# Optimization experiments

Hardware: AMD Instinct MI355X
Metric: run time of the kernel (lower is better)

The kernel has to match this reference:

```python
import jax, jax.numpy as jnp
import numpy as np
import math

DEPTH = 3
NUM_GRAPHS = 8
BN_EPS = 1e-5
POOL_RATIO = 0.5


def _gcn(A, x, W, b):
    # GCNConv(improved=True): A_hat = A + 2*I; out = D^-1/2 A_hat D^-1/2 (x W) + b
    n = A.shape[0]
    A_hat = A + 2.0 * jnp.eye(n, dtype=A.dtype)
    deg = A_hat.sum(axis=1)
    d = jnp.where(deg > 0, jax.lax.rsqrt(deg), 0.0)
    return d[:, None] * (A_hat @ (d[:, None] * (x @ W))) + b


def _bn_eval(x, g, b):
    # BatchNorm1d in eval mode with running_mean=0, running_var=1
    return x * (g / jnp.sqrt(1.0 + BN_EPS)) + b


def _forward(x, edge_index, batch, conv0_w, conv0_b, down_w, down_b, pool_w,
             up_w, up_b, lins_w, lins_b, bn_g, bn_b, out_w, out_b):
    n0 = x.shape[0]
    # dense weighted adjacency A[dst, src] += 1 (duplicates sum, same as scatter-add MP)
    A = jnp.zeros((n0, n0), x.dtype).at[edge_index[1], edge_index[0]].add(1.0)

    # ---- GraphUNet (eval mode: dropout p=0.92 is identity) ----
    h = jax.nn.relu(_gcn(A, x, conv0_w, conv0_b))
    xs, As, perms = [h], [A], []
    for i in range(DEPTH):
        n = A.shape[0]
        eye = jnp.eye(n, dtype=A.dtype)
        S = A + eye                       # add_self_loops(weight=1)
        A2 = (S @ S) * (1.0 - eye)        # spspmm then remove_self_loops
        # TopKPooling: score = tanh((x.w)/||w||), keep top ceil(0.5*n) nodes
        score = jnp.tanh((h @ pool_w[i]) / jnp.linalg.norm(pool_w[i]))
        k = math.ceil(POOL_RATIO * n)
        _, perm = jax.lax.top_k(score, k)
        h = h[perm] * score[perm][:, None]
        A = A2[perm][:, perm]             # filter_adj
        h = jax.nn.relu(_gcn(A, h, down_w[i], down_b[i]))
        if i < DEPTH - 1:
            xs.append(h)
            As.append(A)
        perms.append(perm)
    for i in range(DEPTH):
        j = DEPTH - 1 - i
        res, Aj, perm = xs[j], As[j], perms[j]
        up = jnp.zeros_like(res).at[perm].set(h)
        h = res + up                      # sum_res=True skip connection
        h = _gcn(Aj, h, up_w[i], up_b[i])
        if i < DEPTH - 1:
            h = jax.nn.relu(h)

    # ---- global_add_pool + BN/Linear/tanh head ----
    g = jax.ops.segment_sum(h, batch, num_segments=NUM_GRAPHS)
    for i in range(3):
        g = _bn_eval(g, bn_g[i], bn_b[i])
        g = jnp.tanh(g @ lins_w[i] + lins_b[i])
    g = _bn_eval(g, bn_g[3], bn_b[3])
    return g @ out_w + out_b


def setup_inputs() -> dict:
    key = jax.random.key(0)
    ks = jax.random.split(key, 20)
    N, F, H, O, E = 4096, 64, 128, 32, 65536
    s = 0.05
    x = jax.random.normal(ks[0], (N, F), jnp.float32)
    src = jax.random.randint(ks[1], (E,), 0, N)
    dst = jax.random.randint(ks[2], (E,), 0, N)
    edge_index = jnp.stack([jnp.concatenate([src, dst]),
                            jnp.concatenate([dst, src])]).astype(jnp.int32)
    batch = jnp.sort(jax.random.randint(ks[3], (N,), 0, NUM_GRAPHS)).astype(jnp.int32)
    return {
        "x": x,
        "edge_index": edge_index,
        "batch": batch,
        "conv0_w": jax.random.normal(ks[4], (F, H), jnp.float32) * s,
        "conv0_b": jnp.zeros((H,), jnp.float32),
        "down_w": jax.random.normal(ks[5], (DEPTH, H, H), jnp.float32) * s,
        "down_b": jnp.zeros((DEPTH, H), jnp.float32),
        "pool_w": jax.random.normal(ks[6], (DEPTH, H), jnp.float32),
        "up_w": jax.random.normal(ks[7], (DEPTH, H, H), jnp.float32) * s,
        "up_b": jnp.zeros((DEPTH, H), jnp.float32),
        "lins_w": jax.random.normal(ks[8], (3, H, H), jnp.float32) * s,
        "lins_b": jnp.zeros((3, H), jnp.float32),
        "bn_g": jnp.ones((4, H), jnp.float32),
        "bn_b": jnp.zeros((4, H), jnp.float32),
        "out_w": jax.random.normal(ks[9], (H, O), jnp.float32) * s,
        "out_b": jnp.zeros((O,), jnp.float32),
    }


def reference(x, edge_index, batch, conv0_w, conv0_b, down_w, down_b, pool_w,
              up_w, up_b, lins_w, lins_b, bn_g, bn_b, out_w, out_b):
    return _forward(x, edge_index, batch, conv0_w, conv0_b, down_w, down_b,
                    pool_w, up_w, up_b, lins_w, lins_b, bn_g, bn_b, out_w, out_b)
```

## Files before the change

kernel.cpp:

```cpp
#include <hip/hip_runtime.h>
#include <math.h>

#define H 128
#define NG 8

typedef __attribute__((ext_vector_type(8))) short bf16x8;
typedef __attribute__((ext_vector_type(8))) unsigned short ushort8;
typedef __attribute__((ext_vector_type(4))) float f32x4;

static __device__ __forceinline__ float b2f(unsigned short u) {
  union { unsigned int i; float f; } v;
  v.i = ((unsigned int)u) << 16;
  return v.f;
}
static __device__ __forceinline__ unsigned short f2b(float f) {
  return (unsigned short)(__float_as_uint(f) >> 16);
}

__global__ void k_hist(const int* __restrict__ ei, int E, int* __restrict__ cnt) {
  int e = blockIdx.x * 256 + threadIdx.x;
  if (e >= E) return;
  atomicAdd(&cnt[ei[E + e]], 1);
}

__global__ __launch_bounds__(1024) void k_scan(const int* __restrict__ cnt,
                                               int* __restrict__ rowptr,
                                               float* __restrict__ dv, int n) {
  __shared__ int sums[1024];
  int tid = threadIdx.x;
  int base = tid * 4;
  int v0 = 0, v1 = 0, v2 = 0, v3 = 0;
  if (base < n) { v0 = cnt[base]; v1 = cnt[base + 1]; v2 = cnt[base + 2]; v3 = cnt[base + 3]; }
  int s = v0 + v1 + v2 + v3;
  sums[tid] = s;
  __syncthreads();
  for (int off = 1; off < 1024; off <<= 1) {
    int t = (tid >= off) ? sums[tid - off] : 0;
    __syncthreads();
    sums[tid] += t;
    __syncthreads();
  }
  int excl = sums[tid] - s;
  if (base < n) {
    rowptr[base] = excl;
    rowptr[base + 1] = excl + v0;
    rowptr[base + 2] = excl + v0 + v1;
    rowptr[base + 3] = excl + v0 + v1 + v2;
    dv[base] = rsqrtf((float)v0 + 2.0f);
    dv[base + 1] = rsqrtf((float)v1 + 2.0f);
    dv[base + 2] = rsqrtf((float)v2 + 2.0f);
    dv[base + 3] = rsqrtf((float)v3 + 2.0f);
  }
  if (tid == 1023) rowptr[n] = sums[1023];
}

__global__ void k_fill(const int* __restrict__ ei, int E, const int* __restrict__ rowptr,
                       int* __restrict__ cursor, int* __restrict__ colidx) {
  int e = blockIdx.x * 256 + threadIdx.x;
  if (e >= E) return;
  int r = ei[E + e], c = ei[e];
  int p = atomicAdd(&cursor[r], 1);
  colidx[rowptr[r] + p] = c;
}

__global__ void k_deg(const float* __restrict__ A, int n, float* __restrict__ dv) {
  int row = blockIdx.x * (blockDim.x >> 6) + (threadIdx.x >> 6);
  int lane = threadIdx.x & 63;
  if (row >= n) return;
  float s = 0.f;
  const float* arow = A + (size_t)row * n;
  for (int j = lane; j < n; j += 64) s += arow[j];
#pragma unroll
  for (int o = 32; o > 0; o >>= 1) s += __shfl_down(s, o);
  if (lane == 0) dv[row] = rsqrtf(s + 2.0f);
}

template <int MODE, int RS>
__global__ __launch_bounds__(256) void k_xw(const float* __restrict__ X,
                                            const float* __restrict__ W,
                                            const float* __restrict__ dv,
                                            const int* __restrict__ idx,
                                            const float* __restrict__ aux,
                                            float* __restrict__ Y, int n, int F) {
  __shared__ float Xs[64][36];
  __shared__ float Ws[32][132];
  __shared__ int ridx[64];
  __shared__ float rscl[64];
  int tid = threadIdx.x;
  int rowBase = blockIdx.x * 64;
  if (MODE == 1) {
    if (tid < 64) {
      int pp = idx[rowBase + tid];
      ridx[tid] = pp;
      rscl[tid] = aux[pp];
    }
  } else if (MODE == 2) {
    if (tid < 64) ridx[tid] = idx[rowBase + tid];
  }
  if (MODE != 0) __syncthreads();
  int r0 = (tid >> 5) << 3;
  int c0 = (tid & 31) << 2;
  float acc[8][4] = {};
  for (int k0 = 0; k0 < F; k0 += 32) {
#pragma unroll
    for (int it = 0, e = tid; it < 8; ++it, e += 256) {
      int ii = e >> 5, kk = e & 31;
      int gk = k0 + kk;
      float v;
      if (MODE == 0) {
        v = X[(size_t)(rowBase + ii) * F + gk];
      } else if (MODE == 1) {
        v = X[(size_t)ridx[ii] * F + gk] * rscl[ii];
      } else {
        v = X[(size_t)(rowBase + ii) * F + gk];
        int iv = ridx[ii];
        if (iv >= 0) v += aux[(size_t)iv * H + gk];
      }
      Xs[ii][kk] = v;
    }
#pragma unroll
    for (int it = 0, e = tid; it < 4; ++it, e += 256) {
      int kk = e >> 5, cc4 = e & 31;
      *(float4*)&Ws[kk][cc4 << 2] = *(const float4*)&W[(size_t)(k0 + kk) * H + (cc4 << 2)];
    }
    __syncthreads();
#pragma unroll
    for (int kk = 0; kk < 32; kk += 4) {
      float4 a4[8], w4[4];
#pragma unroll
      for (int i = 0; i < 8; ++i) a4[i] = *(const float4*)&Xs[r0 + i][kk];
#pragma unroll
      for (int s = 0; s < 4; ++s) w4[s] = *(const float4*)&Ws[kk + s][c0];
#pragma unroll
      for (int i = 0; i < 8; ++i) {
        float av[4] = {a4[i].x, a4[i].y, a4[i].z, a4[i].w};
#pragma unroll
        for (int s = 0; s < 4; ++s) {
          float wv[4] = {w4[s].x, w4[s].y, w4[s].z, w4[s].w};
#pragma unroll
          for (int j = 0; j < 4; ++j) acc[i][j] = fmaf(av[s], wv[j], acc[i][j]);
        }
      }
    }
    __syncthreads();
  }
#pragma unroll
  for (int i = 0; i < 8; ++i) {
    int row = rowBase + r0 + i;
    float d = RS ? rsqrtf(dv[row] + 2.0f) : dv[row];
    *(float4*)&Y[(size_t)row * H + c0] =
        make_float4(d * acc[i][0], d * acc[i][1], d * acc[i][2], d * acc[i][3]);
  }
}

__global__ void k_spmm_fin(const int* __restrict__ rowptr, const int* __restrict__ colidx,
                           const float* __restrict__ Y, const float* __restrict__ dv,
                           const float* __restrict__ bias, float* __restrict__ Out,
                           int n, int relu) {
  int row = blockIdx.x * 4 + (threadIdx.x >> 6);
  int lane = threadIdx.x & 63;
  if (row >= n) return;
  int s = rowptr[row], e = rowptr[row + 1];
  int c2 = lane * 2;
  float a0 = 0.f, a1 = 0.f;
  int i = s;
  for (; i + 1 < e; i += 2) {
    int cA = colidx[i], cB = colidx[i + 1];
    float2 yA = *(const float2*)&Y[(size_t)cA * H + c2];
    float2 yB = *(const float2*)&Y[(size_t)cB * H + c2];
    a0 += yA.x + yB.x;
    a1 += yA.y + yB.y;
  }
  if (i < e) {
    int c = colidx[i];
    float2 y = *(const float2*)&Y[(size_t)c * H + c2];
    a0 += y.x;
    a1 += y.y;
  }
  float d = dv[row];
  float2 yr = *(const float2*)&Y[(size_t)row * H + c2];
  float v0 = d * (a0 + 2.0f * yr.x) + bias[c2];
  float v1 = d * (a1 + 2.0f * yr.y) + bias[c2 + 1];
  if (relu) { v0 = fmaxf(v0, 0.f); v1 = fmaxf(v1, 0.f); }
  float2 o = make_float2(v0, v1);
  *(float2*)&Out[(size_t)row * H + c2] = o;
}

__global__ __launch_bounds__(256) void k_ata_rows(const int* __restrict__ rowptr,
                                                  const int* __restrict__ colidx,
                                                  const int* __restrict__ perm,
                                                  const int* __restrict__ inv,
                                                  unsigned short* __restrict__ Ab,
                                                  float* __restrict__ dv, int kdim) {
  __shared__ int acc[2048];
  __shared__ int wsum[4];
  int i = blockIdx.x;
  int tid = threadIdx.x;
  for (int j = tid; j < kdim; j += 256) acc[j] = 0;
  __syncthreads();
  int p = perm[i];
  int s = rowptr[p], e = rowptr[p + 1];
  int deg = e - s;
  int wave = tid >> 6, lane = tid & 63;
  for (int q = wave; q <= deg; q += 4) {
    int kn = (q < deg) ? colidx[s + q] : p;
    int s2 = rowptr[kn], e2 = rowptr[kn + 1];
    for (int idx = s2 + lane; idx <= e2; idx += 64) {
      int j = (idx < e2) ? colidx[idx] : kn;
      int ii = inv[j];
      if (ii >= 0) atomicAdd(&acc[ii], 1);
    }
  }
  __syncthreads();
  int rs = 0;
  {
    int j0 = tid * 8;
    ushort8 v;
#pragma unroll
    for (int q = 0; q < 8; ++q) {
      int j = j0 + q;
      int c = (j == i) ? 0 : acc[j];
      rs += c;
      v[q] = f2b((float)c);
    }
    *(ushort8*)&Ab[(size_t)i * kdim + j0] = v;
  }
#pragma unroll
  for (int o = 32; o > 0; o >>= 1) rs += __shfl_down(rs, o);
  if (lane == 0) wsum[wave] = rs;
  __syncthreads();
  if (tid == 0) dv[i] = rsqrtf((float)(wsum[0] + wsum[1] + wsum[2] + wsum[3]) + 2.0f);
}

__global__ __launch_bounds__(256) void k_ata_mfma_g(const unsigned short* __restrict__ Ab,
                                                    const int* __restrict__ perm,
                                                    float* __restrict__ PartC,
                                                    int n, int k, int KC) {
  __shared__ __align__(16) unsigned short As[64][64];
  __shared__ __align__(16) unsigned short Bs[64][64];
  __shared__ int pr[64], pc[64];
  int tid = threadIdx.x;
  int w = tid >> 6, ln = tid & 63;
  int l15 = ln & 15, l4 = ln >> 4;
  int br = blockIdx.y, bc = blockIdx.x;
  if (tid < 64) pr[tid] = perm[br * 64 + tid];
  else if (tid < 128) pc[tid - 64] = perm[bc * 64 + (tid - 64)];
  __syncthreads();
  f32x4 acc[4] = {};
  int k0s = blockIdx.z * KC;
  for (int k0 = k0s; k0 < k0s + KC; k0 += 64) {
#pragma unroll
    for (int it = 0; it < 2; ++it) {
      int e = tid + it * 256;
      int row = e >> 3, ch = e & 7;
      int sch = (ch ^ (row & 7)) * 8;
      int base = k0 + ch * 8;
      {
        int p = pr[row];
        ushort8 v = *(const ushort8*)&Ab[(size_t)p * n + base];
#pragma unroll
        for (int q = 0; q < 8; ++q)
          if (base + q == p) v[q] = f2b(b2f(v[q]) + 1.0f);
        *(ushort8*)&As[row][sch] = v;
      }
      {
        int p = pc[row];
        ushort8 v = *(const ushort8*)&Ab[(size_t)p * n + base];
#pragma unroll
        for (int q = 0; q < 8; ++q)
          if (base + q == p) v[q] = f2b(b2f(v[q]) + 1.0f);
        *(ushort8*)&Bs[row][sch] = v;
      }
    }
    __syncthreads();
#pragma unroll
    for (int s = 0; s < 2; ++s) {
      int arow = w * 16 + l15;
      bf16x8 af = *(const bf16x8*)&As[arow][((s * 4 + l4) ^ (arow & 7)) * 8];
#pragma unroll
      for (int f = 0; f < 4; ++f) {
        int brow = f * 16 + l15;
        bf16x8 bfr = *(const bf16x8*)&Bs[brow][((s * 4 + l4) ^ (brow & 7)) * 8];
        acc[f] = __builtin_amdgcn_mfma_f32_16x16x32_bf16(af, bfr, acc[f], 0, 0, 0);
      }
    }
    __syncthreads();
  }
  float* out = PartC + (size_t)blockIdx.z * k * k;
#pragma unroll
  for (int f = 0; f < 4; ++f) {
#pragma unroll
    for (int r = 0; r < 4; ++r) {
      int gi = br * 64 + w * 16 + l4 * 4 + r;
      int gj = bc * 64 + f * 16 + l15;
      out[(size_t)gi * k + gj] = acc[f][r];
    }
  }
}

__global__ __launch_bounds__(256) void k_ata_fin(const float* __restrict__ PartC,
                                                 float* __restrict__ C,
                                                 float* __restrict__ rowsum, int k) {
  __shared__ float wsum[4];
  int gi = blockIdx.x;
  int tid = threadIdx.x;
  int j4 = tid * 4;
  size_t stride = (size_t)k * k;
  size_t off = (size_t)gi * k + j4;
  float4 s = *(const float4*)&PartC[off];
#pragma unroll
  for (int z = 1; z < 4; ++z) {
    float4 p = *(const float4*)&PartC[z * stride + off];
    s.x += p.x; s.y += p.y; s.z += p.z; s.w += p.w;
  }
  if (gi >= j4 && gi < j4 + 4) ((float*)&s)[gi - j4] = 0.0f;
  *(float4*)&C[off] = s;
  float part = s.x + s.y + s.z + s.w;
  int lane = tid & 63, wave = tid >> 6;
#pragma unroll
  for (int o = 32; o > 0; o >>= 1) part += __shfl_down(part, o);
  if (lane == 0) wsum[wave] = part;
  __syncthreads();
  if (tid == 0) rowsum[gi] = wsum[0] + wsum[1] + wsum[2] + wsum[3];
}

__global__ void k_cvt_split(const float* __restrict__ Y, unsigned short* __restrict__ YT, int n) {
  int c = blockIdx.x;
  for (int k0 = threadIdx.x * 8; k0 < n; k0 += 256 * 8) {
    ushort8 hi, lo;
#pragma unroll
    for (int q = 0; q < 8; ++q) {
      float v = Y[(size_t)(k0 + q) * H + c];
      unsigned short h = f2b(v);
      hi[q] = h;
      lo[q] = f2b(v - b2f(h));
    }
    *(ushort8*)&YT[(size_t)c * (2 * n) + k0] = hi;
    *(ushort8*)&YT[(size_t)c * (2 * n) + n + k0] = lo;
  }
}

__global__ __launch_bounds__(256) void k_gcn_mfma(const unsigned short* __restrict__ A,
                                                  const unsigned short* __restrict__ YT,
                                                  float* __restrict__ Part, int n, int VK) {
  __shared__ __align__(16) unsigned short As[64][64];
  __shared__ __align__(16) unsigned short Bs[128][64];
  int tid = threadIdx.x;
  int w = tid >> 6, ln = tid & 63;
  int l15 = ln & 15, l4 = ln >> 4;
  int rowBase = blockIdx.x * 64;
  float* out = Part + (size_t)blockIdx.y * n * H;
  f32x4 acc[8] = {};
  int vk0s = blockIdx.y * VK;
  for (int vk0 = vk0s; vk0 < vk0s + VK; vk0 += 64) {
    int ka = vk0 & (n - 1);
#pragma unroll
    for (int it = 0; it < 2; ++it) {
      int e = tid + it * 256;
      int row = e >> 3, ch = e & 7;
      int sch = (ch ^ (row & 7)) * 8;
      *(ushort8*)&As[row][sch] = *(const ushort8*)&A[(size_t)(rowBase + row) * n + ka + ch * 8];
    }
#pragma unroll
    for (int it = 0; it < 4; ++it) {
      int e = tid + it * 256;
      int row = e >> 3, ch = e & 7;
      int sch = (ch ^ (row & 7)) * 8;
      *(ushort8*)&Bs[row][sch] = *(const ushort8*)&YT[(size_t)row * (2 * n) + vk0 + ch * 8];
    }
    __syncthreads();
#pragma unroll
    for (int s = 0; s < 2; ++s) {
      int arow = w * 16 + l15;
      bf16x8 af = *(const bf16x8*)&As[arow][((s * 4 + l4) ^ (arow & 7)) * 8];
#pragma unroll
      for (int f = 0; f < 8; ++f) {
        int brow = f * 16 + l15;
        bf16x8 bfr = *(const bf16x8*)&Bs[brow][((s * 4 + l4) ^ (brow & 7)) * 8];
        acc[f] = __builtin_amdgcn_mfma_f32_16x16x32_bf16(af, bfr, acc[f], 0, 0, 0);
      }
    }
    __syncthreads();
  }
#pragma unroll
  for (int f = 0; f < 8; ++f) {
#pragma unroll
    for (int r = 0; r < 4; ++r) {
      int row = rowBase + w * 16 + l4 * 4 + r;
      out[(size_t)row * H + f * 16 + l15] = acc[f][r];
    }
  }
}

__global__ __launch_bounds__(256) void k_ata_sk(const float* __restrict__ A,
                                                const int* __restrict__ perm,
                                                float* __restrict__ C, int n, int k, int CK) {
  int bc = blockIdx.x, br = blockIdx.y;
  if (br > bc) return;
  __shared__ float As[64][36];
  __shared__ float Bs[64][36];
  __shared__ int pr[64], pc[64];
  int tid = threadIdx.x;
  if (tid < 64) pr[tid] = perm[br * 64 + tid];
  else if (tid < 128) pc[tid - 64] = perm[bc * 64 + (tid - 64)];
  __syncthreads();
  int ty = tid >> 4;
  int tx = tid & 15;
  float acc[4][4] = {};
  int k0s = blockIdx.z * CK;
  for (int k0 = k0s; k0 < k0s + CK; k0 += 32) {
#pragma unroll
    for (int it = 0, e = tid; it < 8; ++it, e += 256) {
      int ii = e >> 5, kk = e & 31;
      int gk = k0 + kk;
      int p = pr[ii];
      As[ii][kk] = A[(size_t)p * n + gk] + ((p == gk) ? 1.0f : 0.0f);
      p = pc[ii];
      Bs[ii][kk] = A[(size_t)p * n + gk] + ((p == gk) ? 1.0f : 0.0f);
    }
    __syncthreads();
#pragma unroll
    for (int kk = 0; kk < 32; kk += 4) {
      float4 a4[4], b4[4];
#pragma unroll
      for (int i = 0; i < 4; ++i) a4[i] = *(const float4*)&As[ty + 16 * i][kk];
#pragma unroll
      for (int j = 0; j < 4; ++j) b4[j] = *(const float4*)&Bs[tx + 16 * j][kk];
#pragma unroll
      for (int i = 0; i < 4; ++i) {
        float av[4] = {a4[i].x, a4[i].y, a4[i].z, a4[i].w};
#pragma unroll
        for (int j = 0; j < 4; ++j) {
          float bv[4] = {b4[j].x, b4[j].y, b4[j].z, b4[j].w};
#pragma unroll
          for (int s = 0; s < 4; ++s) acc[i][j] = fmaf(av[s], bv[s], acc[i][j]);
        }
      }
    }
    __syncthreads();
  }
  bool diag = (br == bc);
#pragma unroll
  for (int i = 0; i < 4; ++i) {
    int gi = br * 64 + ty + 16 * i;
#pragma unroll
    for (int j = 0; j < 4; ++j) {
      int gj = bc * 64 + tx + 16 * j;
      if (gi == gj) continue;
      float v = acc[i][j];
      atomicAdd(&C[(size_t)gi * k + gj], v);
      if (!diag) atomicAdd(&C[(size_t)gj * k + gi], v);
    }
  }
}

__global__ __launch_bounds__(256) void k_gcn_part(const float* __restrict__ A,
                                                  const float* __restrict__ Y,
                                                  float* __restrict__ Part,
                                                  int n, int KC) {
  __shared__ float As[64][36];
  __shared__ float Ys[32][132];
  int tid = threadIdx.x;
  int r0 = (tid >> 5) << 3;
  int c0 = (tid & 31) << 2;
  size_t rowBase = (size_t)blockIdx.x * 64;
  int k0s = blockIdx.y * KC;
  float* out = Part + (size_t)blockIdx.y * n * H;
  float acc[8][4] = {};
  for (int k0 = k0s; k0 < k0s + KC; k0 += 32) {
#pragma unroll
    for (int it = 0, e = tid; it < 8; ++it, e += 256) {
      int ii = e >> 5, kk = e & 31;
      As[ii][kk] = A[(rowBase + ii) * (size_t)n + k0 + kk];
    }
#pragma unroll
    for (int it = 0, e = tid; it < 4; ++it, e += 256) {
      int kk = e >> 5, cc4 = e & 31;
      *(float4*)&Ys[kk][cc4 << 2] = *(const float4*)&Y[(size_t)(k0 + kk) * H + (cc4 << 2)];
    }
    __syncthreads();
#pragma unroll
    for (int kk = 0; kk < 32; kk += 4) {
      float4 a4[8], y4[4];
#pragma unroll
      for (int i = 0; i < 8; ++i) a4[i] = *(const float4*)&As[r0 + i][kk];
#pragma unroll
      for (int s = 0; s < 4; ++s) y4[s] = *(const float4*)&Ys[kk + s][c0];
#pragma unroll
      for (int i = 0; i < 8; ++i) {
        float av[4] = {a4[i].x, a4[i].y, a4[i].z, a4[i].w};
#pragma unroll
        for (int s = 0; s < 4; ++s) {
          float yv[4] = {y4[s].x, y4[s].y, y4[s].z, y4[s].w};
#pragma unroll
          for (int j = 0; j < 4; ++j) acc[i][j] = fmaf(av[s], yv[j], acc[i][j]);
        }
      }
    }
    __syncthreads();
  }
#pragma unroll
  for (int i = 0; i < 8; ++i) {
    size_t row = rowBase + r0 + i;
    *(float4*)&out[row * H + c0] = make_float4(acc[i][0], acc[i][1], acc[i][2], acc[i][3]);
  }
}

template <int RS>
__global__ void k_gcn_fin(const float* __restrict__ Part, const float* __restrict__ Y,
                          const float* __restrict__ dv, const float* __restrict__ bias,
                          float* __restrict__ Out, int n, int nch, int relu) {
  int i4 = blockIdx.x * 256 + threadIdx.x;
  if (i4 * 4 >= n * H) return;
  int row = i4 >> 5, c4 = (i4 & 31) * 4;
  size_t stride = (size_t)n * H;
  float4 s = *(const float4*)&Part[i4 * 4];
  for (int c = 1; c < nch; ++c) {
    float4 p = *(const float4*)&Part[c * stride + i4 * 4];
    s.x += p.x; s.y += p.y; s.z += p.z; s.w += p.w;
  }
  float4 y = *(const float4*)&Y[i4 * 4];
  float d = RS ? rsqrtf(dv[row] + 2.0f) : dv[row];
  float4 v;
  v.x = d * (s.x + 2.0f * y.x) + bias[c4];
  v.y = d * (s.y + 2.0f * y.y) + bias[c4 + 1];
  v.z = d * (s.z + 2.0f * y.z) + bias[c4 + 2];
  v.w = d * (s.w + 2.0f * y.w) + bias[c4 + 3];
  if (relu) {
    v.x = fmaxf(v.x, 0.f); v.y = fmaxf(v.y, 0.f);
    v.z = fmaxf(v.z, 0.f); v.w = fmaxf(v.w, 0.f);
  }
  *(float4*)&Out[i4 * 4] = v;
}

__global__ void k_score(const float* __restrict__ h, const float* __restrict__ w,
                        float* __restrict__ score, int n) {
  __shared__ float wn;
  int tid = threadIdx.x;
  if (tid < 64) {
    float s = w[tid] * w[tid] + w[tid + 64] * w[tid + 64];
#pragma unroll
    for (int o = 32; o > 0; o >>= 1) s += __shfl_down(s, o);
    if (tid == 0) wn = sqrtf(s);
  }
  __syncthreads();
  int row = blockIdx.x * 4 + (tid >> 6);
  int lane = tid & 63;
  if (row >= n) return;
  float s = h[(size_t)row * H + lane] * w[lane] + h[(size_t)row * H + lane + 64] * w[lane + 64];
#pragma unroll
  for (int o = 32; o > 0; o >>= 1) s += __shfl_down(s, o);
  if (lane == 0) score[row] = tanhf(s / wn);
}

static __device__ __forceinline__ void ce_(unsigned long long& x, unsigned long long& y, bool asc) {
  if ((x < y) != asc) { unsigned long long t = x; x = y; y = t; }
}
static __device__ __forceinline__ unsigned long long pick_(unsigned long long a,
                                                           unsigned long long b,
                                                           bool lower, bool asc) {
  unsigned long long lo = (a < b) ? a : b;
  unsigned long long hi = (a < b) ? b : a;
  return (lower == asc) ? lo : hi;
}

template <int LOGN>
__global__ __launch_bounds__(1024) void k_topk(const float* __restrict__ score,
                                               int* __restrict__ perm,
                                               int* __restrict__ inv) {
  const int n = 1 << LOGN;
  __shared__ unsigned long long lds[1 << LOGN];
  int t = threadIdx.x;
  int e0 = t * 4;
  unsigned long long key[4];
#pragma unroll
  for (int j = 0; j < 4; ++j) {
    unsigned u = __float_as_uint(score[e0 + j]);
    u = (u & 0x80000000u) ? ~u : (u | 0x80000000u);
    u = ~u;
    key[j] = (((unsigned long long)u) << 32) | (unsigned)(e0 + j);
  }
  ce_(key[0], key[1], true);
  ce_(key[2], key[3], false);
  for (int size = 4; size <= n; size <<= 1) {
    bool asc = ((e0 & size) == 0);
    for (int stride = size >> 1; stride >= 256; stride >>= 1) {
#pragma unroll
      for (int j = 0; j < 4; ++j) lds[e0 + j] = key[j];
      __syncthreads();
      bool lower = ((e0 & stride) == 0);
#pragma unroll
      for (int j = 0; j < 4; ++j)
        key[j] = pick_(key[j], lds[(e0 + j) ^ stride], lower, asc);
      __syncthreads();
    }
    int s0 = ((size >> 1) < 256) ? (size >> 1) : 128;
    for (int stride = s0; stride >= 4; stride >>= 1) {
      int m = stride >> 2;
      bool lower = ((t & m) == 0);
#pragma unroll
      for (int j = 0; j < 4; ++j) {
        unsigned long long o = __shfl_xor(key[j], m, 64);
        key[j] = pick_(key[j], o, lower, asc);
      }
    }
    ce_(key[0], key[2], asc);
    ce_(key[1], key[3], asc);
    ce_(key[0], key[1], asc);
    ce_(key[2], key[3], asc);
  }
  int kk = n >> 1;
#pragma unroll
  for (int j = 0; j < 4; ++j) {
    int e = e0 + j;
    int idx = (int)(key[j] & 0xffffffffu);
    if (e < kk) perm[e] = idx;
    if (inv) inv[idx] = (e < kk) ? e : -1;
  }
}

__global__ void k_segsum(const float* __restrict__ h, const int* __restrict__ batch,
                         float* __restrict__ g, int n) {
  int c = threadIdx.x;
  int r0 = blockIdx.x * 32;
  int rend = min(r0 + 32, n);
  float acc = 0.f;
  int cur = batch[r0];
  for (int r = r0; r < rend; ++r) {
    int b = batch[r];
    if (b != cur) { atomicAdd(&g[cur * H + c], acc); acc = 0.f; cur = b; }
    acc += h[(size_t)r * H + c];
  }
  atomicAdd(&g[cur * H + c], acc);
}

__global__ __launch_bounds__(256) void k_head(const float* __restrict__ g,
    const float* __restrict__ lins_w, const float* __restrict__ lins_b,
    const float* __restrict__ bn_g, const float* __restrict__ bn_b,
    const float* __restrict__ out_w, const float* __restrict__ out_b,
    float* __restrict__ out) {
  __shared__ float a[NG * H], b[NG * H];
  int tid = threadIdx.x;
  const float inv = 1.0f / sqrtf(1.0f + 1e-5f);
  for (int i = tid; i < NG * H; i += 256) a[i] = g[i];
  __syncthreads();
  for (int L = 0; L < 3; ++L) {
    for (int i = tid; i < NG * H; i += 256) {
      int c = i & 127;
      b[i] = a[i] * (bn_g[L * H + c] * inv) + bn_b[L * H + c];
    }
    __syncthreads();
    for (int i = tid; i < NG * H; i += 256) {
      int r = i >> 7, c = i & 127;
      float s = lins_b[L * H + c];
      for (int k2 = 0; k2 < H; ++k2) s += b[r * H + k2] * lins_w[(size_t)L * H * H + k2 * H + c];
      a[i] = tanhf(s);
    }
    __syncthreads();
  }
  for (int i = tid; i < NG * H; i += 256) {
    int c = i & 127;
    b[i] = a[i] * (bn_g[3 * H + c] * inv) + bn_b[3 * H + c];
  }
  __syncthreads();
  for (int i = tid; i < NG * 32; i += 256) {
    int r = i >> 5, o = i & 31;
    float s = out_b[o];
    for (int k2 = 0; k2 < H; ++k2) s += b[r * H + k2] * out_w[k2 * 32 + o];
    out[i] = s;
  }
}

extern "C" void kernel_launch(void* const* d_in, const int* in_sizes, int n_in,
                              void* d_out, int out_size, void* d_ws, size_t ws_size,
                              hipStream_t stream) {
  const float* x       = (const float*)d_in[0];
  const int*   ei      = (const int*)d_in[1];
  const int*   batch   = (const int*)d_in[2];
  const float* conv0_w = (const float*)d_in[3];
  const float* conv0_b = (const float*)d_in[4];
  const float* down_w  = (const float*)d_in[5];
  const float* down_b  = (const float*)d_in[6];
  const float* pool_w  = (const float*)d_in[7];
  const float* up_w    = (const float*)d_in[8];
  const float* up_b    = (const float*)d_in[9];
  const float* lins_w  = (const float*)d_in[10];
  const float* lins_b  = (const float*)d_in[11];
  const float* bn_g    = (const float*)d_in[12];
  const float* bn_b    = (const float*)d_in[13];
  const float* out_w   = (const float*)d_in[14];
  const float* out_b   = (const float*)d_in[15];
  int E = in_sizes[1] / 2;

  char* p = (char*)d_ws;
  auto alloc = [&](size_t bytes) {
    char* r = p;
    p += (bytes + 255) & ~(size_t)255;
    return r;
  };
  unsigned short* A1b  = (unsigned short*)alloc((size_t)2048 * 2048 * 2);
  unsigned short* YT   = (unsigned short*)alloc((size_t)128 * 4096 * 2);
  float*          A2m  = (float*)alloc((size_t)1024 * 1024 * 4);
  float*          A3   = (float*)alloc((size_t)512 * 512 * 4);
  float*          part = (float*)alloc((size_t)16 * 1024 * 1024 * 4);
  int* cnt    = (int*)alloc(4096 * 4);
  int* cursor = (int*)alloc(4096 * 4);
  int* rowptr = (int*)alloc(4100 * 4);
  int* colidx = (int*)alloc((size_t)E * 4);
  int* inv0   = (int*)alloc(4096 * 4);
  int* inv1   = (int*)alloc(2048 * 4);
  int* inv2   = (int*)alloc(1024 * 4);
  float* dv0  = (float*)alloc(4096 * 4);
  float* dv1  = (float*)alloc(2048 * 4);
  float* dv2  = (float*)alloc(1024 * 4);
  float* dv3  = (float*)alloc(512 * 4);
  int* perm0  = (int*)alloc(2048 * 4);
  int* perm1  = (int*)alloc(1024 * 4);
  int* perm2  = (int*)alloc(512 * 4);
  float* score = (float*)alloc(4096 * 4);
  float* h0 = (float*)alloc((size_t)4096 * H * 4);
  float* h1 = (float*)alloc((size_t)2048 * H * 4);
  float* h2 = (float*)alloc((size_t)1024 * H * 4);
  float* h3 = (float*)alloc((size_t)512 * H * 4);
  float* t2 = (float*)alloc((size_t)4096 * H * 4);
  float* hu = (float*)alloc((size_t)4096 * H * 4);
  float* g  = (float*)alloc(NG * H * 4);

  auto gcn = [&](const float* A, const float* Y, const float* dvv, const float* bias,
                 float* Out, int nn, int relu, bool rs) {
    const int nch = 8;
    int KC = nn / nch;
    k_gcn_part<<<dim3(nn / 64, nch), 256, 0, stream>>>(A, Y, part, nn, KC);
    if (rs)
      k_gcn_fin<1><<<nn / 8, 256, 0, stream>>>(part, Y, dvv, bias, Out, nn, nch, relu);
    else
      k_gcn_fin<0><<<nn / 8, 256, 0, stream>>>(part, Y, dvv, bias, Out, nn, nch, relu);
  };
  auto gcn_mfma = [&](const unsigned short* Ab, const float* Y, const float* dvv,
                      const float* bias, float* Out, int nn, int relu) {
    k_cvt_split<<<128, 256, 0, stream>>>(Y, YT, nn);
    k_gcn_mfma<<<dim3(nn / 64, 16), 256, 0, stream>>>(Ab, YT, part, nn, (2 * nn) / 16);
    k_gcn_fin<0><<<nn / 8, 256, 0, stream>>>(part, Y, dvv, bias, Out, nn, 16, relu);
  };

  hipMemsetAsync(cnt, 0, 4096 * 4, stream);
  hipMemsetAsync(cursor, 0, 4096 * 4, stream);
  k_hist<<<(E + 255) / 256, 256, 0, stream>>>(ei, E, cnt);
  k_scan<<<1, 1024, 0, stream>>>(cnt, rowptr, dv0, 4096);
  k_fill<<<(E + 255) / 256, 256, 0, stream>>>(ei, E, rowptr, cursor, colidx);

  k_xw<0, 0><<<4096 / 64, 256, 0, stream>>>(x, conv0_w, dv0, nullptr, nullptr, t2, 4096, 64);
  k_spmm_fin<<<1024, 256, 0, stream>>>(rowptr, colidx, t2, dv0, conv0_b, h0, 4096, 1);

  k_score<<<1024, 256, 0, stream>>>(h0, pool_w, score, 4096);
  k_topk<12><<<1, 1024, 0, stream>>>(score, perm0, inv0);
  k_ata_rows<<<2048, 256, 0, stream>>>(rowptr, colidx, perm0, inv0, A1b, dv1, 2048);
  k_xw<1, 0><<<2048 / 64, 256, 0, stream>>>(h0, down_w, dv1, perm0, score, t2, 2048, 128);
  gcn_mfma(A1b, t2, dv1, down_b, h1, 2048, 1);

  k_score<<<512, 256, 0, stream>>>(h1, pool_w + H, score, 2048);
  k_topk<11><<<1, 512, 0, stream>>>(score, perm1, inv1);
  k_ata_mfma_g<<<dim3(16, 16, 4), 256, 0, stream>>>(A1b, perm1, part, 2048, 1024, 512);
  k_ata_fin<<<1024, 256, 0, stream>>>(part, A2m, dv2, 1024);
  k_xw<1, 1><<<1024 / 64, 256, 0, stream>>>(h1, down_w + (size_t)H * H, dv2, perm1, score, t2, 1024, 128);
  gcn(A2m, t2, dv2, down_b + H, h2, 1024, 1, true);

  k_score<<<256, 256, 0, stream>>>(h2, pool_w + 2 * H, score, 1024);
  k_topk<10><<<1, 256, 0, stream>>>(score, perm2, inv2);
  hipMemsetAsync(A3, 0, (size_t)512 * 512 * 4, stream);
  k_ata_sk<<<dim3(8, 8, 8), 256, 0, stream>>>(A2m, perm2, A3, 1024, 512, 128);
  k_deg<<<512 / 4, 256, 0, stream>>>(A3, 512, dv3);
  k_xw<1, 0><<<512 / 64, 256, 0, stream>>>(h2, down_w + (size_t)2 * H * H, dv3, perm2, score, t2, 512, 128);
  gcn(A3, t2, dv3, down_b + 2 * H, h3, 512, 1, false);

  k_xw<2, 1><<<1024 / 64, 256, 0, stream>>>(h2, up_w, dv2, inv2, h3, t2, 1024, 128);
  gcn(A2m, t2, dv2, up_b, hu, 1024, 1, true);

  k_xw<2, 0><<<2048 / 64, 256, 0, stream>>>(h1, up_w + (size_t)H * H, dv1, inv1, hu, t2, 2048, 128);
  gcn_mfma(A1b, t2, dv1, up_b + H, hu, 2048, 1);

  k_xw<2, 0><<<4096 / 64, 256, 0, stream>>>(h0, up_w + (size_t)2 * H * H, dv0, inv0, hu, t2, 4096, 128);
  k_spmm_fin<<<1024, 256, 0, stream>>>(rowptr, colidx, t2, dv0, up_b + 2 * H, hu, 4096, 0);

  hipMemsetAsync(g, 0, NG * H * 4, stream);
  k_segsum<<<4096 / 32, 128, 0, stream>>>(hu, batch, g, 4096);
  k_head<<<1, 256, 0, stream>>>(g, lins_w, lins_b, bn_g, bn_b, out_w, out_b, (float*)d_out);
}
```

Baseline: 512.0 us.

## Fuse score into GCN epilogues, emit bf16 split in xw, replace atomic ATA with partials

```diff
diff --git a/kernel.cpp b/kernel.cpp
--- a/kernel.cpp
+++ b/kernel.cpp
@@ -63,25 +63,15 @@
   colidx[rowptr[r] + p] = c;
 }
 
-__global__ void k_deg(const float* __restrict__ A, int n, float* __restrict__ dv) {
-  int row = blockIdx.x * (blockDim.x >> 6) + (threadIdx.x >> 6);
-  int lane = threadIdx.x & 63;
-  if (row >= n) return;
-  float s = 0.f;
-  const float* arow = A + (size_t)row * n;
-  for (int j = lane; j < n; j += 64) s += arow[j];
-#pragma unroll
-  for (int o = 32; o > 0; o >>= 1) s += __shfl_down(s, o);
-  if (lane == 0) dv[row] = rsqrtf(s + 2.0f);
-}
-
-template <int MODE, int RS>
+template <int MODE, int RS, int EMIT>
 __global__ __launch_bounds__(256) void k_xw(const float* __restrict__ X,
                                             const float* __restrict__ W,
                                             const float* __restrict__ dv,
                                             const int* __restrict__ idx,
                                             const float* __restrict__ aux,
-                                            float* __restrict__ Y, int n, int F) {
+                                            float* __restrict__ Y,
+                                            unsigned short* __restrict__ YT,
+                                            int n, int F) {
   __shared__ float Xs[64][36];
   __shared__ float Ws[32][132];
   __shared__ int ridx[64];
@@ -144,21 +134,53 @@
     }
     __syncthreads();
   }
+  float vout[8][4];
 #pragma unroll
   for (int i = 0; i < 8; ++i) {
     int row = rowBase + r0 + i;
     float d = RS ? rsqrtf(dv[row] + 2.0f) : dv[row];
+#pragma unroll
+    for (int j = 0; j < 4; ++j) vout[i][j] = d * acc[i][j];
     *(float4*)&Y[(size_t)row * H + c0] =
-        make_float4(d * acc[i][0], d * acc[i][1], d * acc[i][2], d * acc[i][3]);
-  }
-}
-
+        make_float4(vout[i][0], vout[i][1], vout[i][2], vout[i][3]);
+  }
+  if (EMIT) {
+#pragma unroll
+    for (int j = 0; j < 4; ++j) {
+      ushort8 hi, lo;
+#pragma unroll
+      for (int i = 0; i < 8; ++i) {
+        float v = vout[i][j];
+        unsigned short hh = f2b(v);
+        hi[i] = hh;
+        lo[i] = f2b(v - b2f(hh));
+      }
+      int c = c0 + j;
+      *(ushort8*)&YT[(size_t)c * (2 * n) + rowBase + r0] = hi;
+      *(ushort8*)&YT[(size_t)c * (2 * n) + n + rowBase + r0] = lo;
+    }
+  }
+}
+
+template <int SCORE>
 __global__ void k_spmm_fin(const int* __restrict__ rowptr, const int* __restrict__ colidx,
                            const float* __restrict__ Y, const float* __restrict__ dv,
                            const float* __restrict__ bias, float* __restrict__ Out,
+                           const float* __restrict__ w, float* __restrict__ score,
                            int n, int relu) {
-  int row = blockIdx.x * 4 + (threadIdx.x >> 6);
-  int lane = threadIdx.x & 63;
+  __shared__ float wn;
+  int tid = threadIdx.x;
+  if (SCORE) {
+    if (tid < 64) {
+      float s = w[tid] * w[tid] + w[tid + 64] * w[tid + 64];
+#pragma unroll
+      for (int o = 32; o > 0; o >>= 1) s += __shfl_down(s, o);
+      if (tid == 0) wn = sqrtf(s);
+    }
+    __syncthreads();
+  }
+  int row = blockIdx.x * 4 + (tid >> 6);
+  int lane = tid & 63;
   if (row >= n) return;
   int s = rowptr[row], e = rowptr[row + 1];
   int c2 = lane * 2;
@@ -182,8 +204,13 @@
   float v0 = d * (a0 + 2.0f * yr.x) + bias[c2];
   float v1 = d * (a1 + 2.0f * yr.y) + bias[c2 + 1];
   if (relu) { v0 = fmaxf(v0, 0.f); v1 = fmaxf(v1, 0.f); }
-  float2 o = make_float2(v0, v1);
-  *(float2*)&Out[(size_t)row * H + c2] = o;
+  *(float2*)&Out[(size_t)row * H + c2] = make_float2(v0, v1);
+  if (SCORE) {
+    float sc = v0 * w[c2] + v1 * w[c2 + 1];
+#pragma unroll
+    for (int o = 32; o > 0; o >>= 1) sc += __shfl_down(sc, o);
+    if (lane == 0) score[row] = tanhf(sc / wn);
+  }
 }
 
 __global__ __launch_bounds__(256) void k_ata_rows(const int* __restrict__ rowptr,
@@ -298,9 +325,68 @@
   }
 }
 
-__global__ __launch_bounds__(256) void k_ata_fin(const float* __restrict__ PartC,
-                                                 float* __restrict__ C,
-                                                 float* __restrict__ rowsum, int k) {
+__global__ __launch_bounds__(256) void k_ata_sk_part(const float* __restrict__ A,
+                                                     const int* __restrict__ perm,
+                                                     float* __restrict__ PartC,
+                                                     int n, int k, int CK) {
+  int bc = blockIdx.x, br = blockIdx.y;
+  __shared__ float As[64][36];
+  __shared__ float Bs[64][36];
+  __shared__ int pr[64], pc[64];
+  int tid = threadIdx.x;
+  if (tid < 64) pr[tid] = perm[br * 64 + tid];
+  else if (tid < 128) pc[tid - 64] = perm[bc * 64 + (tid - 64)];
+  __syncthreads();
+  int ty = tid >> 4;
+  int tx = tid & 15;
+  float acc[4][4] = {};
+  int k0s = blockIdx.z * CK;
+  for (int k0 = k0s; k0 < k0s + CK; k0 += 32) {
+#pragma unroll
+    for (int it = 0, e = tid; it < 8; ++it, e += 256) {
+      int ii = e >> 5, kk = e & 31;
+      int gk = k0 + kk;
+      int p = pr[ii];
+      As[ii][kk] = A[(size_t)p * n + gk] + ((p == gk) ? 1.0f : 0.0f);
+      p = pc[ii];
+      Bs[ii][kk] = A[(size_t)p * n + gk] + ((p == gk) ? 1.0f : 0.0f);
+    }
+    __syncthreads();
+#pragma unroll
+    for (int kk = 0; kk < 32; kk += 4) {
+      float4 a4[4], b4[4];
+#pragma unroll
+      for (int i = 0; i < 4; ++i) a4[i] = *(const float4*)&As[ty + 16 * i][kk];
+#pragma unroll
+      for (int j = 0; j < 4; ++j) b4[j] = *(const float4*)&Bs[tx + 16 * j][kk];
+#pragma unroll
+      for (int i = 0; i < 4; ++i) {
+        float av[4] = {a4[i].x, a4[i].y, a4[i].z, a4[i].w};
+#pragma unroll
+        for (int j = 0; j < 4; ++j) {
+          float bv[4] = {b4[j].x, b4[j].y, b4[j].z, b4[j].w};
+#pragma unroll
+          for (int s = 0; s < 4; ++s) acc[i][j] = fmaf(av[s], bv[s], acc[i][j]);
+        }
+      }
+    }
+    __syncthreads();
+  }
+  float* out = PartC + (size_t)blockIdx.z * k * k;
+#pragma unroll
+  for (int i = 0; i < 4; ++i) {
+    int gi = br * 64 + ty + 16 * i;
+#pragma unroll
+    for (int j = 0; j < 4; ++j) {
+      int gj = bc * 64 + tx + 16 * j;
+      out[(size_t)gi * k + gj] = acc[i][j];
+    }
+  }
+}
+
+template <int NCH>
+__global__ void k_ata_fin(const float* __restrict__ PartC, float* __restrict__ C,
+                          float* __restrict__ rowsum, int k) {
   __shared__ float wsum[4];
   int gi = blockIdx.x;
   int tid = threadIdx.x;
@@ -309,7 +395,7 @@
   size_t off = (size_t)gi * k + j4;
   float4 s = *(const float4*)&PartC[off];
 #pragma unroll
-  for (int z = 1; z < 4; ++z) {
+  for (int z = 1; z < NCH; ++z) {
     float4 p = *(const float4*)&PartC[z * stride + off];
     s.x += p.x; s.y += p.y; s.z += p.z; s.w += p.w;
   }
@@ -321,22 +407,11 @@
   for (int o = 32; o > 0; o >>= 1) part += __shfl_down(part, o);
   if (lane == 0) wsum[wave] = part;
   __syncthreads();
-  if (tid == 0) rowsum[gi] = wsum[0] + wsum[1] + wsum[2] + wsum[3];
-}
-
-__global__ void k_cvt_split(const float* __restrict__ Y, unsigned short* __restrict__ YT, int n) {
-  int c = blockIdx.x;
-  for (int k0 = threadIdx.x * 8; k0 < n; k0 += 256 * 8) {
-    ushort8 hi, lo;
-#pragma unroll
-    for (int q = 0; q < 8; ++q) {
-      float v = Y[(size_t)(k0 + q) * H + c];
-      unsigned short h = f2b(v);
-      hi[q] = h;
-      lo[q] = f2b(v - b2f(h));
-    }
-    *(ushort8*)&YT[(size_t)c * (2 * n) + k0] = hi;
-    *(ushort8*)&YT[(size_t)c * (2 * n) + n + k0] = lo;
+  if (tid == 0) {
+    int nw = blockDim.x >> 6;
+    float t = 0.f;
+    for (int q = 0; q < nw; ++q) t += wsum[q];
+    rowsum[gi] = t;
   }
 }
 
@@ -392,68 +467,6 @@
   }
 }
 
-__global__ __launch_bounds__(256) void k_ata_sk(const float* __restrict__ A,
-                                                const int* __restrict__ perm,
-                                                float* __restrict__ C, int n, int k, int CK) {
-  int bc = blockIdx.x, br = blockIdx.y;
-  if (br > bc) return;
-  __shared__ float As[64][36];
-  __shared__ float Bs[64][36];
-  __shared__ int pr[64], pc[64];
-  int tid = threadIdx.x;
-  if (tid < 64) pr[tid] = perm[br * 64 + tid];
-  else if (tid < 128) pc[tid - 64] = perm[bc * 64 + (tid - 64)];
-  __syncthreads();
-  int ty = tid >> 4;
-  int tx = tid & 15;
-  float acc[4][4] = {};
-  int k0s = blockIdx.z * CK;
-  for (int k0 = k0s; k0 < k0s + CK; k0 += 32) {
-#pragma unroll
-    for (int it = 0, e = tid; it < 8; ++it, e += 256) {
-      int ii = e >> 5, kk = e & 31;
-      int gk = k0 + kk;
-      int p = pr[ii];
-      As[ii][kk] = A[(size_t)p * n + gk] + ((p == gk) ? 1.0f : 0.0f);
-      p = pc[ii];
-      Bs[ii][kk] = A[(size_t)p * n + gk] + ((p == gk) ? 1.0f : 0.0f);
-    }
-    __syncthreads();
-#pragma unroll
-    for (int kk = 0; kk < 32; kk += 4) {
-      float4 a4[4], b4[4];
-#pragma unroll
-      for (int i = 0; i < 4; ++i) a4[i] = *(const float4*)&As[ty + 16 * i][kk];
-#pragma unroll
-      for (int j = 0; j < 4; ++j) b4[j] = *(const float4*)&Bs[tx + 16 * j][kk];
-#pragma unroll
-      for (int i = 0; i < 4; ++i) {
-        float av[4] = {a4[i].x, a4[i].y, a4[i].z, a4[i].w};
-#pragma unroll
-        for (int j = 0; j < 4; ++j) {
-          float bv[4] = {b4[j].x, b4[j].y, b4[j].z, b4[j].w};
-#pragma unroll
-          for (int s = 0; s < 4; ++s) acc[i][j] = fmaf(av[s], bv[s], acc[i][j]);
-        }
-      }
-    }
-    __syncthreads();
-  }
-  bool diag = (br == bc);
-#pragma unroll
-  for (int i = 0; i < 4; ++i) {
-    int gi = br * 64 + ty + 16 * i;
-#pragma unroll
-    for (int j = 0; j < 4; ++j) {
-      int gj = bc * 64 + tx + 16 * j;
-      if (gi == gj) continue;
-      float v = acc[i][j];
-      atomicAdd(&C[(size_t)gi * k + gj], v);
-      if (!diag) atomicAdd(&C[(size_t)gj * k + gi], v);
-    }
-  }
-}
-
 __global__ __launch_bounds__(256) void k_gcn_part(const float* __restrict__ A,
                                                   const float* __restrict__ Y,
                                                   float* __restrict__ Part,
@@ -506,12 +519,24 @@
   }
 }
 
-template <int RS>
+template <int RS, int SCORE>
 __global__ void k_gcn_fin(const float* __restrict__ Part, const float* __restrict__ Y,
                           const float* __restrict__ dv, const float* __restrict__ bias,
-                          float* __restrict__ Out, int n, int nch, int relu) {
-  int i4 = blockIdx.x * 256 + threadIdx.x;
-  if (i4 * 4 >= n * H) return;
+                          float* __restrict__ Out,
+                          const float* __restrict__ w, float* __restrict__ score,
+                          int n, int nch, int relu) {
+  __shared__ float wn;
+  int tid = threadIdx.x;
+  if (SCORE) {
+    if (tid < 64) {
+      float s = w[tid] * w[tid] + w[tid + 64] * w[tid + 64];
+#pragma unroll
+      for (int o = 32; o > 0; o >>= 1) s += __shfl_down(s, o);
+      if (tid == 0) wn = sqrtf(s);
+    }
+    __syncthreads();
+  }
+  int i4 = blockIdx.x * 256 + tid;
   int row = i4 >> 5, c4 = (i4 & 31) * 4;
   size_t stride = (size_t)n * H;
   float4 s = *(const float4*)&Part[i4 * 4];
@@ -531,26 +556,12 @@
     v.z = fmaxf(v.z, 0.f); v.w = fmaxf(v.w, 0.f);
   }
   *(float4*)&Out[i4 * 4] = v;
-}
-
-__global__ void k_score(const float* __restrict__ h, const float* __restrict__ w,
-                        float* __restrict__ score, int n) {
-  __shared__ float wn;
-  int tid = threadIdx.x;
-  if (tid < 64) {
-    float s = w[tid] * w[tid] + w[tid + 64] * w[tid + 64];
-#pragma unroll
-    for (int o = 32; o > 0; o >>= 1) s += __shfl_down(s, o);
-    if (tid == 0) wn = sqrtf(s);
-  }
-  __syncthreads();
-  int row = blockIdx.x * 4 + (tid >> 6);
-  int lane = tid & 63;
-  if (row >= n) return;
-  float s = h[(size_t)row * H + lane] * w[lane] + h[(size_t)row * H + lane + 64] * w[lane + 64];
-#pragma unroll
-  for (int o = 32; o > 0; o >>= 1) s += __shfl_down(s, o);
-  if (lane == 0) score[row] = tanhf(s / wn);
+  if (SCORE) {
+    float sc = v.x * w[c4] + v.y * w[c4 + 1] + v.z * w[c4 + 2] + v.w * w[c4 + 3];
+#pragma unroll
+    for (int o = 16; o > 0; o >>= 1) sc += __shfl_down(sc, o, 32);
+    if ((tid & 31) == 0) score[row] = tanhf(sc / wn);
+  }
 }
 
 static __device__ __forceinline__ void ce_(unsigned long long& x, unsigned long long& y, bool asc) {
@@ -726,61 +737,44 @@
   float* hu = (float*)alloc((size_t)4096 * H * 4);
   float* g  = (float*)alloc(NG * H * 4);
 
-  auto gcn = [&](const float* A, const float* Y, const float* dvv, const float* bias,
-                 float* Out, int nn, int relu, bool rs) {
-    const int nch = 8;
-    int KC = nn / nch;
-    k_gcn_part<<<dim3(nn / 64, nch), 256, 0, stream>>>(A, Y, part, nn, KC);
-    if (rs)
-      k_gcn_fin<1><<<nn / 8, 256, 0, stream>>>(part, Y, dvv, bias, Out, nn, nch, relu);
-    else
-      k_gcn_fin<0><<<nn / 8, 256, 0, stream>>>(part, Y, dvv, bias, Out, nn, nch, relu);
-  };
-  auto gcn_mfma = [&](const unsigned short* Ab, const float* Y, const float* dvv,
-                      const float* bias, float* Out, int nn, int relu) {
-    k_cvt_split<<<128, 256, 0, stream>>>(Y, YT, nn);
-    k_gcn_mfma<<<dim3(nn / 64, 16), 256, 0, stream>>>(Ab, YT, part, nn, (2 * nn) / 16);
-    k_gcn_fin<0><<<nn / 8, 256, 0, stream>>>(part, Y, dvv, bias, Out, nn, 16, relu);
-  };
-
-  hipMemsetAsync(cnt, 0, 4096 * 4, stream);
-  hipMemsetAsync(cursor, 0, 4096 * 4, stream);
+  hipMemsetAsync(cnt, 0, 2 * 4096 * 4, stream);
   k_hist<<<(E + 255) / 256, 256, 0, stream>>>(ei, E, cnt);
   k_scan<<<1, 1024, 0, stream>>>(cnt, rowptr, dv0, 4096);
   k_fill<<<(E + 255) / 256, 256, 0, stream>>>(ei, E, rowptr, cursor, colidx);
 
-  k_xw<0, 0><<<4096 / 64, 256, 0, stream>>>(x, conv0_w, dv0, nullptr, nullptr, t2, 4096, 64);
-  k_spmm_fin<<<1024, 256, 0, stream>>>(rowptr, colidx, t2, dv0, conv0_b, h0, 4096, 1);
-
-  k_score<<<1024, 256, 0, stream>>>(h0, pool_w, score, 4096);
+  k_xw<0, 0, 0><<<4096 / 64, 256, 0, stream>>>(x, conv0_w, dv0, nullptr, nullptr, t2, nullptr, 4096, 64);
+  k_spmm_fin<1><<<1024, 256, 0, stream>>>(rowptr, colidx, t2, dv0, conv0_b, h0, pool_w, score, 4096, 1);
+
   k_topk<12><<<1, 1024, 0, stream>>>(score, perm0, inv0);
   k_ata_rows<<<2048, 256, 0, stream>>>(rowptr, colidx, perm0, inv0, A1b, dv1, 2048);
-  k_xw<1, 0><<<2048 / 64, 256, 0, stream>>>(h0, down_w, dv1, perm0, score, t2, 2048, 128);
-  gcn_mfma(A1b, t2, dv1, down_b, h1, 2048, 1);
-
-  k_score<<<512, 256, 0, stream>>>(h1, pool_w + H, score, 2048);
+  k_xw<1, 0, 1><<<2048 / 64, 256, 0, stream>>>(h0, down_w, dv1, perm0, score, t2, YT, 2048, 128);
+  k_gcn_mfma<<<dim3(2048 / 64, 16), 256, 0, stream>>>(A1b, YT, part, 2048, 4096 / 16);
+  k_gcn_fin<0, 1><<<2048 / 8, 256, 0, stream>>>(part, t2, dv1, down_b, h1, pool_w + H, score, 2048, 16, 1);
+
   k_topk<11><<<1, 512, 0, stream>>>(score, perm1, inv1);
   k_ata_mfma_g<<<dim3(16, 16, 4), 256, 0, stream>>>(A1b, perm1, part, 2048, 1024, 512);
-  k_ata_fin<<<1024, 256, 0, stream>>>(part, A2m, dv2, 1024);
-  k_xw<1, 1><<<1024 / 64, 256, 0, stream>>>(h1, down_w + (size_t)H * H, dv2, perm1, score, t2, 1024, 128);
-  gcn(A2m, t2, dv2, down_b + H, h2, 1024, 1, true);
-
-  k_score<<<256, 256, 0, stream>>>(h2, pool_w + 2 * H, score, 1024);
+  k_ata_fin<4><<<1024, 256, 0, stream>>>(part, A2m, dv2, 1024);
+  k_xw<1, 1, 0><<<1024 / 64, 256, 0, stream>>>(h1, down_w + (size_t)H * H, dv2, perm1, score, t2, nullptr, 1024, 128);
+  k_gcn_part<<<dim3(1024 / 64, 8), 256, 0, stream>>>(A2m, t2, part, 1024, 128);
+  k_gcn_fin<1, 1><<<1024 / 8, 256, 0, stream>>>(part, t2, dv2, down_b + H, h2, pool_w + 2 * H, score, 1024, 8, 1);
+
   k_topk<10><<<1, 256, 0, stream>>>(score, perm2, inv2);
-  hipMemsetAsync(A3, 0, (size_t)512 * 512 * 4, stream);
-  k_ata_sk<<<dim3(8, 8, 8), 256, 0, stream>>>(A2m, perm2, A3, 1024, 512, 128);
-  k_deg<<<512 / 4, 256, 0, stream>>>(A3, 512, dv3);
-  k_xw<1, 0><<<512 / 64, 256, 0, stream>>>(h2, down_w + (size_t)2 * H * H, dv3, perm2, score, t2, 512, 128);
-  gcn(A3, t2, dv3, down_b + 2 * H, h3, 512, 1, false);
-
-  k_xw<2, 1><<<1024 / 64, 256, 0, stream>>>(h2, up_w, dv2, inv2, h3, t2, 1024, 128);
-  gcn(A2m, t2, dv2, up_b, hu, 1024, 1, true);
-
-  k_xw<2, 0><<<2048 / 64, 256, 0, stream>>>(h1, up_w + (size_t)H * H, dv1, inv1, hu, t2, 2048, 128);
-  gcn_mfma(A1b, t2, dv1, up_b + H, hu, 2048, 1);
-
-  k_xw<2, 0><<<4096 / 64, 256, 0, stream>>>(h0, up_w + (size_t)2 * H * H, dv0, inv0, hu, t2, 4096, 128);
-  k_spmm_fin<<<1024, 256, 0, stream>>>(rowptr, colidx, t2, dv0, up_b + 2 * H, hu, 4096, 0);
+  k_ata_sk_part<<<dim3(8, 8, 8), 256, 0, stream>>>(A2m, perm2, part, 1024, 512, 128);
+  k_ata_fin<8><<<512, 128, 0, stream>>>(part, A3, dv3, 512);
+  k_xw<1, 1, 0><<<512 / 64, 256, 0, stream>>>(h2, down_w + (size_t)2 * H * H, dv3, perm2, score, t2, nullptr, 512, 128);
+  k_gcn_part<<<dim3(512 / 64, 8), 256, 0, stream>>>(A3, t2, part, 512, 64);
+  k_gcn_fin<1, 0><<<512 / 8, 256, 0, stream>>>(part, t2, dv3, down_b + 2 * H, h3, nullptr, nullptr, 512, 8, 1);
+
+  k_xw<2, 1, 0><<<1024 / 64, 256, 0, stream>>>(h2, up_w, dv2, inv2, h3, t2, nullptr, 1024, 128);
+  k_gcn_part<<<dim3(1024 / 64, 8), 256, 0, stream>>>(A2m, t2, part, 1024, 128);
+  k_gcn_fin<1, 0><<<1024 / 8, 256, 0, stream>>>(part, t2, dv2, up_b, hu, nullptr, nullptr, 1024, 8, 1);
+
+  k_xw<2, 0, 1><<<2048 / 64, 256, 0, stream>>>(h1, up_w + (size_t)H * H, dv1, inv1, hu, t2, YT, 2048, 128);
+  k_gcn_mfma<<<dim3(2048 / 64, 16), 256, 0, stream>>>(A1b, YT, part, 2048, 4096 / 16);
+  k_gcn_fin<0, 0><<<2048 / 8, 256, 0, stream>>>(part, t2, dv1, up_b + H, hu, nullptr, nullptr, 2048, 16, 1);
+
+  k_xw<2, 0, 0><<<4096 / 64, 256, 0, stream>>>(h0, up_w + (size_t)2 * H * H, dv0, inv0, hu, t2, nullptr, 4096, 128);
+  k_spmm_fin<0><<<1024, 256, 0, stream>>>(rowptr, colidx, t2, dv0, up_b + 2 * H, hu, nullptr, nullptr, 4096, 0);
 
   hipMemsetAsync(g, 0, NG * H * 4, stream);
   k_segsum<<<4096 / 32, 128, 0, stream>>>(hu, batch, g, 4096);
```

New measurement: 522.9 us. 1.02x slower.
